# Performance work log

Measured on AMD Instinct MI355X. Metric: run time of the kernel, lower is better.

The kernel has to match this reference:

```python
import jax, jax.numpy as jnp
import numpy as np

N = 20000
E = 320000
F_IN = 256
NHID = 64
H1 = 8
H2 = 1
NUM_CLASSES = 40
NEG_SLOPE = 0.2


def setup_inputs() -> dict:
    key = jax.random.key(0)
    ks = jax.random.split(key, 11)
    glorot = lambda k, shape: jax.random.normal(k, shape, jnp.float32) * jnp.sqrt(2.0 / (shape[0] + shape[-1]))
    x = jax.random.normal(ks[0], (N, F_IN), jnp.float32)
    edge_index = jax.random.randint(ks[1], (2, E), 0, N, jnp.int64)
    W1 = glorot(ks[2], (F_IN, H1 * NHID))
    att_src1 = glorot(ks[3], (H1, NHID))
    att_dst1 = glorot(ks[4], (H1, NHID))
    b1 = jnp.zeros((H1 * NHID,), jnp.float32)
    W2 = glorot(ks[5], (H1 * NHID, H2 * NUM_CLASSES))
    att_src2 = glorot(ks[6], (H2, NUM_CLASSES))
    att_dst2 = glorot(ks[7], (H2, NUM_CLASSES))
    b2 = jnp.zeros((NUM_CLASSES,), jnp.float32)
    return {"x": x, "edge_index": edge_index, "W1": W1, "att_src1": att_src1,
            "att_dst1": att_dst1, "b1": b1, "W2": W2, "att_src2": att_src2,
            "att_dst2": att_dst2, "b2": b2}


def gat_conv(x, src, dst, W, a_src, a_dst, bias, concat):
    # x: [N, F_in], src/dst: [E'] (self-loops already appended)
    H, C = a_src.shape
    h = (x @ W).reshape(N, H, C)                       # [N,H,C]
    alpha_src = jnp.sum(h * a_src, axis=-1)            # [N,H]
    alpha_dst = jnp.sum(h * a_dst, axis=-1)            # [N,H]
    e = jax.nn.leaky_relu(alpha_src[src] + alpha_dst[dst], NEG_SLOPE)  # [E',H]
    # segment softmax over incoming edges of each dst node
    emax = jax.lax.stop_gradient(jax.ops.segment_max(e, dst, num_segments=N))
    ee = jnp.exp(e - emax[dst])
    denom = jax.ops.segment_sum(ee, dst, num_segments=N)
    alpha = ee / (denom[dst] + 1e-16)                  # [E',H]
    out = jax.ops.segment_sum(alpha[:, :, None] * h[src], dst, num_segments=N)  # [N,H,C]
    out = out.reshape(N, H * C) if concat else out.mean(axis=1)
    return out + bias


def reference(x, edge_index, W1, att_src1, att_dst1, b1, W2, att_src2, att_dst2, b2):
    # PyG GATConv adds self-loops by default
    loops = jnp.arange(N, dtype=edge_index.dtype)
    src = jnp.concatenate([edge_index[0], loops])
    dst = jnp.concatenate([edge_index[1], loops])
    h = gat_conv(x, src, dst, W1, att_src1, att_dst1, b1, concat=True)   # [N, H1*NHID]
    h = jax.nn.elu(h)
    out = gat_conv(h, src, dst, W2, att_src2, att_dst2, b2, concat=False)  # [N, NUM_CLASSES]
    return jax.nn.log_softmax(out, axis=1)
```

## Files before the change

### kernel.cpp

```cpp
#include <hip/hip_runtime.h>
#include <hip/hip_bf16.h>
#include <math.h>

#define N_NODES 20000
#define MPAD 20096
#define N_EDGES 320000
#define EP (N_EDGES + N_NODES)
#define F_IN 256
#define NHID 64
#define H1 8
#define D1 512
#define NCLS 40
#define NEG_SLOPE 0.2f
#define MAXD 128

typedef __attribute__((ext_vector_type(8))) short bf16x8;
typedef __attribute__((ext_vector_type(4))) float f32x4;

__device__ __forceinline__ float wave_max(float v) {
#pragma unroll
  for (int o = 32; o > 0; o >>= 1) v = fmaxf(v, __shfl_xor(v, o));
  return v;
}
__device__ __forceinline__ float wave_sum(float v) {
#pragma unroll
  for (int o = 32; o > 0; o >>= 1) v += __shfl_xor(v, o);
  return v;
}
__device__ __forceinline__ float bf2f(unsigned short u) {
  union { unsigned int i; float f; } c; c.i = ((unsigned int)u) << 16; return c.f;
}
__device__ __forceinline__ unsigned short f2bf(float f) {
  union { float f; unsigned int i; } c; c.f = f;
  unsigned int x = c.i;
  return (unsigned short)((x + 0x7fffu + ((x >> 16) & 1u)) >> 16);
}
__device__ __forceinline__ float asf(unsigned int u) {
  union { unsigned int i; float f; } c; c.i = u; return c.f;
}
__device__ __forceinline__ float lrelu(float x) { return x > 0.f ? x : NEG_SLOPE * x; }

__device__ __forceinline__ void gload16(const void* g, void* l) {
  __builtin_amdgcn_global_load_lds((const __attribute__((address_space(1))) void*)g,
                                   (__attribute__((address_space(3))) void*)l, 16, 0, 0);
}

#define PB_CONV 2512
#define PB_TW1  (PB_CONV + 32)
#define PB_TW2  (PB_TW1 + 96)
#define PB_ZERO (PB_TW2 + 157)
#define PB_PAD  (PB_ZERO + 24)
__global__ __launch_bounds__(256) void prep_kernel(const float* __restrict__ x,
                                                   const float* __restrict__ W1,
                                                   const float* __restrict__ W2,
                                                   unsigned short* __restrict__ xb,
                                                   unsigned short* __restrict__ wb1t,
                                                   unsigned short* __restrict__ wb2t,
                                                   int* __restrict__ deg,
                                                   int* __restrict__ cursor,
                                                   unsigned short* __restrict__ out1b) {
  __shared__ float tsh[64][65];
  int bid = blockIdx.x;
  int t = threadIdx.x;
  if (bid < PB_CONV) {
    size_t base = ((size_t)bid * 256 + t) * 8;
    int row = (int)(base >> 8);
    ushort4 o0, o1;
    if (row < N_NODES) {
      float4 v0 = *(const float4*)&x[base];
      float4 v1 = *(const float4*)&x[base + 4];
      o0 = make_ushort4(f2bf(v0.x), f2bf(v0.y), f2bf(v0.z), f2bf(v0.w));
      o1 = make_ushort4(f2bf(v1.x), f2bf(v1.y), f2bf(v1.z), f2bf(v1.w));
    } else {
      o0 = make_ushort4(0, 0, 0, 0); o1 = o0;
    }
    *(ushort4*)&xb[base] = o0;
    *(ushort4*)&xb[base + 4] = o1;
  } else if (bid < PB_TW1) {
    int b2 = bid - PB_CONV;
    int bk = b2 & 3, bn = b2 >> 2;
    int tr = t >> 4, tc4 = (t & 15) * 4;
#pragma unroll
    for (int i = 0; i < 4; ++i) {
      int k = i * 16 + tr;
      float4 v = *(const float4*)&W1[(size_t)(bk * 64 + k) * D1 + bn * 64 + tc4];
      tsh[k][tc4] = v.x; tsh[k][tc4 + 1] = v.y; tsh[k][tc4 + 2] = v.z; tsh[k][tc4 + 3] = v.w;
    }
    __syncthreads();
#pragma unroll
    for (int i = 0; i < 4; ++i) {
      int n = i * 16 + tr;
      ushort4 o = make_ushort4(f2bf(tsh[tc4][n]), f2bf(tsh[tc4 + 1][n]),
                               f2bf(tsh[tc4 + 2][n]), f2bf(tsh[tc4 + 3][n]));
      *(ushort4*)&wb1t[(size_t)(bn * 64 + n) * F_IN + bk * 64 + tc4] = o;
    }
  } else if (bid < PB_TW2) {
    int idx = (bid - PB_TW1) * 256 + t;
    int c = idx >> 9, k = idx & 511;
    wb2t[idx] = f2bf((c < NCLS) ? W2[(size_t)k * NCLS + c] : 0.f);
  } else if (bid < PB_ZERO) {
    int idx = (bid - PB_TW2) * 256 + t;
    if (idx < N_NODES) deg[idx] = 0;
    else if (idx < 2 * N_NODES) cursor[idx - N_NODES] = 0;
  } else {
    int idx = (bid - PB_ZERO) * 256 + t;
    uint4 z = make_uint4(0, 0, 0, 0);
    *(uint4*)((char*)out1b + (size_t)N_NODES * D1 * 2 + (size_t)idx * 16) = z;
  }
}

__global__ void count_deg(const int* __restrict__ ei, int* __restrict__ deg) {
  int e = blockIdx.x * blockDim.x + threadIdx.x;
  if (e >= EP) return;
  int dst = (e < N_EDGES) ? ei[N_EDGES + e] : (e - N_EDGES);
  atomicAdd(&deg[dst], 1);
}

#define SCAN_T 256
#define SCAN_CHUNK 79
__global__ void scan_kernel(const int* __restrict__ deg, int* __restrict__ offsets) {
  __shared__ int sums[SCAN_T];
  int t = threadIdx.x;
  int lo = t * SCAN_CHUNK;
  int hi = min(lo + SCAN_CHUNK, N_NODES);
  int s = 0;
  for (int i = lo; i < hi; ++i) s += deg[i];
  sums[t] = s;
  __syncthreads();
  if (t == 0) {
    int run = 0;
    for (int i = 0; i < SCAN_T; ++i) { int v = sums[i]; sums[i] = run; run += v; }
  }
  __syncthreads();
  int run = sums[t];
  for (int i = lo; i < hi; ++i) { offsets[i] = run; run += deg[i]; }
  if (hi == N_NODES) offsets[N_NODES] = run;
}

__global__ void scatter_edges(const int* __restrict__ ei, const int* __restrict__ offsets,
                              int* __restrict__ cursor, int* __restrict__ edge_src) {
  int e = blockIdx.x * blockDim.x + threadIdx.x;
  if (e >= EP) return;
  int src, dst;
  if (e < N_EDGES) { src = ei[e]; dst = ei[N_EDGES + e]; }
  else             { src = dst = e - N_EDGES; }
  int pos = offsets[dst] + atomicAdd(&cursor[dst], 1);
  edge_src[pos] = src;
}

__global__ __launch_bounds__(256) void gemm1_mfma(const unsigned short* __restrict__ xb,
                                                  const unsigned short* __restrict__ wb1t,
                                                  const float* __restrict__ a_src,
                                                  const float* __restrict__ a_dst,
                                                  unsigned short* __restrict__ h1b,
                                                  float* __restrict__ asrc,
                                                  float* __restrict__ adst) {
  __shared__ unsigned short As[128 * 32];
  __shared__ unsigned short Bs[128 * 32];
  int tid = threadIdx.x;
  int w = tid >> 6, lane = tid & 63;
  int bn = blockIdx.x & 3, bm = blockIdx.x >> 2;
  int row0 = bm * 128, col0 = bn * 128;
  int wr = w >> 1, wc = w & 1;
  int cl = lane & 15, hi = lane >> 4;
  f32x4 acc[4][4] = {};
  for (int k0 = 0; k0 < F_IN; k0 += 32) {
#pragma unroll
    for (int c = 0; c < 2; ++c) {
      int slot = c * 256 + tid;
      int r = slot >> 2;
      int q = (slot & 3) ^ ((slot >> 3) & 3);
      gload16(xb + (size_t)(row0 + r) * F_IN + k0 + q * 8, (char*)As + (c * 256 + w * 64) * 16);
      gload16(wb1t + (size_t)(col0 + r) * F_IN + k0 + q * 8, (char*)Bs + (c * 256 + w * 64) * 16);
    }
    __syncthreads();
    bf16x8 a[4], b[4];
#pragma unroll
    for (int m = 0; m < 4; ++m) {
      int r = wr * 64 + m * 16 + cl;
      a[m] = *(const bf16x8*)&As[r * 32 + ((hi ^ ((r >> 1) & 3)) << 3)];
    }
#pragma unroll
    for (int n = 0; n < 4; ++n) {
      int r = wc * 64 + n * 16 + cl;
      b[n] = *(const bf16x8*)&Bs[r * 32 + ((hi ^ ((r >> 1) & 3)) << 3)];
    }
#pragma unroll
    for (int m = 0; m < 4; ++m)
#pragma unroll
      for (int n = 0; n < 4; ++n)
        acc[m][n] = __builtin_amdgcn_mfma_f32_16x16x32_bf16(a[m], b[n], acc[m][n], 0, 0, 0);
    __syncthreads();
  }
  int head = bn * 2 + wc;
  float asv[4], adv[4];
#pragma unroll
  for (int n = 0; n < 4; ++n) {
    asv[n] = a_src[head * 64 + n * 16 + cl];
    adv[n] = a_dst[head * 64 + n * 16 + cl];
  }
#pragma unroll
  for (int m = 0; m < 4; ++m) {
#pragma unroll
    for (int r = 0; r < 4; ++r) {
      int grow = row0 + wr * 64 + m * 16 + hi * 4 + r;
      float ps = acc[m][0][r] * asv[0] + acc[m][1][r] * asv[1] +
                 acc[m][2][r] * asv[2] + acc[m][3][r] * asv[3];
      float pd = acc[m][0][r] * adv[0] + acc[m][1][r] * adv[1] +
                 acc[m][2][r] * adv[2] + acc[m][3][r] * adv[3];
#pragma unroll
      for (int o = 8; o > 0; o >>= 1) { ps += __shfl_xor(ps, o); pd += __shfl_xor(pd, o); }
      if (grow < N_NODES) {
#pragma unroll
        for (int n = 0; n < 4; ++n)
          h1b[(size_t)grow * D1 + col0 + wc * 64 + n * 16 + cl] = f2bf(acc[m][n][r]);
        if (cl == 0) { asrc[grow * H1 + head] = ps; adst[grow * H1 + head] = pd; }
      }
    }
  }
}

__global__ __launch_bounds__(128) void agg1_kernel(const int* __restrict__ offsets,
                                                   const int* __restrict__ edge_src,
                                                   const float* __restrict__ asrc,
                                                   const float* __restrict__ adst,
                                                   const unsigned short* __restrict__ h1b,
                                                   const float* __restrict__ b1,
                                                   unsigned short* __restrict__ out1b) {
  __shared__ float alphaT[MAXD][H1 + 1];
  __shared__ int   lsoff[MAXD];
  __shared__ float red[2][8];
  __shared__ float minv[2][8];
  __shared__ float accs[2][D1];
  int n = blockIdx.x;
  int t = threadIdx.x;
  int w = t >> 6, lane = t & 63;
  int base = offsets[n];
  int deg = offsets[n + 1] - base;
  int degc = min(deg, MAXD);

  for (int e = t; e < degc; e += 128) lsoff[e] = edge_src[base + e] << 10;
  __syncthreads();

  int h = t & 7;
  int et = t >> 3;
  float advv = adst[n * H1 + h];
  float m = -INFINITY;
  for (int e = et; e < degc; e += 16) {
    int s = lsoff[e] >> 10;
    float ev = lrelu(asrc[s * H1 + h] + advv);
    alphaT[e][h] = ev;
    m = fmaxf(m, ev);
  }
  for (int e = MAXD + et; e < deg; e += 16)
    m = fmaxf(m, lrelu(asrc[edge_src[base + e] * H1 + h] + advv));
  m = fmaxf(m, __shfl_xor(m, 8));
  m = fmaxf(m, __shfl_xor(m, 16));
  m = fmaxf(m, __shfl_xor(m, 32));
  if (lane < 8) red[w][lane] = m;
  __syncthreads();
  m = fmaxf(red[0][h], red[1][h]);
  float ss = 0.f;
  for (int e = et; e < degc; e += 16) ss += __expf(alphaT[e][h] - m);
  for (int e = MAXD + et; e < deg; e += 16)
    ss += __expf(lrelu(asrc[edge_src[base + e] * H1 + h] + advv) - m);
  ss += __shfl_xor(ss, 8);
  ss += __shfl_xor(ss, 16);
  ss += __shfl_xor(ss, 32);
  __syncthreads();
  if (lane < 8) red[w][lane] = ss;
  __syncthreads();
  float inv = 1.f / (red[0][h] + red[1][h] + 1e-16f);
  if (t < 8) { minv[0][t] = m; minv[1][t] = inv; }
  for (int e = et; e < degc; e += 16)
    alphaT[e][h] = __expf(alphaT[e][h] - m) * inv;
  __syncthreads();

  int myh = lane >> 3;
  const char* hb = (const char*)h1b + lane * 16;
  float acc[8] = {};
  for (int e = w; e < degc; e += 2) {
    float a = alphaT[e][myh];
    uint4 uv = *(const uint4*)(hb + lsoff[e]);
#pragma unroll
    for (int j = 0; j < 4; ++j) {
      unsigned int u = ((const unsigned int*)&uv)[j];
      acc[2 * j]     += a * asf(u << 16);
      acc[2 * j + 1] += a * asf(u & 0xffff0000u);
    }
  }
  if (deg > MAXD) {
    float mh = minv[0][myh], invh = minv[1][myh];
    float advh = adst[n * H1 + myh];
    for (int e = MAXD + w; e < deg; e += 2) {
      int s = edge_src[base + e];
      float a = __expf(lrelu(asrc[s * H1 + myh] + advh) - mh) * invh;
      uint4 uv = *(const uint4*)(hb + ((size_t)s << 10));
#pragma unroll
      for (int j = 0; j < 4; ++j) {
        unsigned int u = ((const unsigned int*)&uv)[j];
        acc[2 * j]     += a * asf(u << 16);
        acc[2 * j + 1] += a * asf(u & 0xffff0000u);
      }
    }
  }
  *(float4*)&accs[w][lane * 8]     = make_float4(acc[0], acc[1], acc[2], acc[3]);
  *(float4*)&accs[w][lane * 8 + 4] = make_float4(acc[4], acc[5], acc[6], acc[7]);
  __syncthreads();

  int c0 = t * 4;
  float4 s0 = *(float4*)&accs[0][c0];
  float4 s1 = *(float4*)&accs[1][c0];
  float4 bv = *(const float4*)&b1[c0];
  float v0 = s0.x + s1.x + bv.x, v1 = s0.y + s1.y + bv.y;
  float v2 = s0.z + s1.z + bv.z, v3 = s0.w + s1.w + bv.w;
  v0 = v0 > 0.f ? v0 : (__expf(v0) - 1.f);
  v1 = v1 > 0.f ? v1 : (__expf(v1) - 1.f);
  v2 = v2 > 0.f ? v2 : (__expf(v2) - 1.f);
  v3 = v3 > 0.f ? v3 : (__expf(v3) - 1.f);
  ushort4 o = make_ushort4(f2bf(v0), f2bf(v1), f2bf(v2), f2bf(v3));
  *(ushort4*)&out1b[(size_t)n * D1 + c0] = o;
}

__global__ __launch_bounds__(256) void gemm2_mfma(const unsigned short* __restrict__ ab,
                                                  const unsigned short* __restrict__ wb2t,
                                                  const float* __restrict__ a_src2,
                                                  const float* __restrict__ a_dst2,
                                                  float* __restrict__ h2,
                                                  float* __restrict__ asrc,
                                                  float* __restrict__ adst) {
  __shared__ unsigned short As[128 * 32];
  __shared__ unsigned short Bs[48 * 32];
  int tid = threadIdx.x;
  int w = tid >> 6, lane = tid & 63;
  int row0 = blockIdx.x * 128;
  int cl = lane & 15, hi = lane >> 4;
  f32x4 acc[2][3] = {};
  for (int k0 = 0; k0 < D1; k0 += 32) {
#pragma unroll
    for (int c = 0; c < 2; ++c) {
      int slot = c * 256 + tid;
      int r = slot >> 2;
      int q = (slot & 3) ^ ((slot >> 3) & 3);
      gload16(ab + (size_t)(row0 + r) * D1 + k0 + q * 8, (char*)As + (c * 256 + w * 64) * 16);
    }
    if (tid < 192) {
      int r = tid >> 2;
      int q = (tid & 3) ^ ((tid >> 3) & 3);
      gload16(wb2t + (size_t)r * D1 + k0 + q * 8, (char*)Bs + w * 64 * 16);
    }
    __syncthreads();
    bf16x8 a[2], b[3];
#pragma unroll
    for (int m = 0; m < 2; ++m) {
      int r = w * 32 + m * 16 + cl;
      a[m] = *(const bf16x8*)&As[r * 32 + ((hi ^ ((r >> 1) & 3)) << 3)];
    }
#pragma unroll
    for (int n = 0; n < 3; ++n) {
      int r = n * 16 + cl;
      b[n] = *(const bf16x8*)&Bs[r * 32 + ((hi ^ ((r >> 1) & 3)) << 3)];
    }
#pragma unroll
    for (int m = 0; m < 2; ++m)
#pragma unroll
      for (int n = 0; n < 3; ++n)
        acc[m][n] = __builtin_amdgcn_mfma_f32_16x16x32_bf16(a[m], b[n], acc[m][n], 0, 0, 0);
    __syncthreads();
  }
  float asv[3], adv[3];
#pragma unroll
  for (int n = 0; n < 3; ++n) {
    int c = n * 16 + cl;
    asv[n] = (c < NCLS) ? a_src2[c] : 0.f;
    adv[n] = (c < NCLS) ? a_dst2[c] : 0.f;
  }
#pragma unroll
  for (int m = 0; m < 2; ++m) {
#pragma unroll
    for (int r = 0; r < 4; ++r) {
      int grow = row0 + w * 32 + m * 16 + hi * 4 + r;
      float ps = acc[m][0][r] * asv[0] + acc[m][1][r] * asv[1] + acc[m][2][r] * asv[2];
      float pd = acc[m][0][r] * adv[0] + acc[m][1][r] * adv[1] + acc[m][2][r] * adv[2];
#pragma unroll
      for (int o = 8; o > 0; o >>= 1) { ps += __shfl_xor(ps, o); pd += __shfl_xor(pd, o); }
      if (grow < N_NODES) {
#pragma unroll
        for (int n = 0; n < 3; ++n) {
          int c = n * 16 + cl;
          if (c < NCLS) h2[(size_t)grow * NCLS + c] = acc[m][n][r];
        }
        if (cl == 0) { asrc[grow] = ps; adst[grow] = pd; }
      }
    }
  }
}

__global__ __launch_bounds__(256) void agg2_kernel(const int* __restrict__ offsets,
                                                   const int* __restrict__ edge_src,
                                                   const float* __restrict__ asrc,
                                                   const float* __restrict__ adst,
                                                   const float* __restrict__ h2,
                                                   const float* __restrict__ b2,
                                                   float* __restrict__ out) {
  __shared__ float lalpha[4][MAXD];
  __shared__ int   lsoff[4][MAXD];
  int w = threadIdx.x >> 6;
  int lane = threadIdx.x & 63;
  int n = blockIdx.x * 4 + w;
  int base = offsets[n];
  int deg = offsets[n + 1] - base;
  int degc = min(deg, MAXD);
  int degp = ((degc + 2) / 3) * 3;

  float advv = adst[n];
  float m = -INFINITY;
  for (int e = lane; e < deg; e += 64) {
    int s = edge_src[base + e];
    float ev = lrelu(asrc[s] + advv);
    if (e < MAXD) { lsoff[w][e] = s * (NCLS * 4); lalpha[w][e] = ev; }
    m = fmaxf(m, ev);
  }
  m = wave_max(m);
  float ssum = 0.f;
  for (int e = lane; e < deg; e += 64) {
    float ev;
    if (e < MAXD) ev = lalpha[w][e];
    else { int s = edge_src[base + e]; ev = lrelu(asrc[s] + advv); }
    ssum += __expf(ev - m);
  }
  float inv = 1.f / (wave_sum(ssum) + 1e-16f);
  for (int e = lane; e < degc; e += 64) lalpha[w][e] = __expf(lalpha[w][e] - m) * inv;
  {
    int e = degc + lane;
    if (e < degp && e < MAXD) { lalpha[w][e] = 0.f; lsoff[w][e] = 0; }
  }

  int esub = lane / 20;
  int cg = lane - esub * 20;
  bool act = esub < 3;
  float ax = 0.f, ay = 0.f;
  const char* hb = (const char*)h2 + cg * 8;
  for (int i = 0; i < degp; i += 3) {
    if (act) {
      int slot = i + esub;
      float a = lalpha[w][slot];
      int so = lsoff[w][slot];
      float2 hv = *(const float2*)(hb + so);
      ax += a * hv.x; ay += a * hv.y;
    }
  }
  for (int e = MAXD + esub; e < deg; e += 3) {
    if (act) {
      int s = edge_src[base + e];
      float a = __expf(lrelu(asrc[s] + advv) - m) * inv;
      float2 hv = *(const float2*)(hb + (size_t)s * (NCLS * 4));
      ax += a * hv.x; ay += a * hv.y;
    }
  }
  float ax1 = __shfl(ax, lane + 20), ax2 = __shfl(ax, lane + 40);
  float ay1 = __shfl(ay, lane + 20), ay2 = __shfl(ay, lane + 40);
  float v0 = -INFINITY, v1 = -INFINITY;
  if (lane < 20) {
    v0 = ax + ax1 + ax2 + b2[2 * cg];
    v1 = ay + ay1 + ay2 + b2[2 * cg + 1];
  }
  float m2 = wave_max(fmaxf(v0, v1));
  float se = wave_sum(lane < 20 ? __expf(v0 - m2) + __expf(v1 - m2) : 0.f);
  if (lane < 20) {
    float ls = logf(se);
    *(float2*)&out[(size_t)n * NCLS + 2 * cg] = make_float2(v0 - m2 - ls, v1 - m2 - ls);
  }
}

extern "C" void kernel_launch(void* const* d_in, const int* in_sizes, int n_in,
                              void* d_out, int out_size, void* d_ws, size_t ws_size,
                              hipStream_t stream) {
  const float* x   = (const float*)d_in[0];
  const int*   ei  = (const int*)d_in[1];
  const float* W1  = (const float*)d_in[2];
  const float* as1 = (const float*)d_in[3];
  const float* ad1 = (const float*)d_in[4];
  const float* b1  = (const float*)d_in[5];
  const float* W2  = (const float*)d_in[6];
  const float* as2 = (const float*)d_in[7];
  const float* ad2 = (const float*)d_in[8];
  const float* b2  = (const float*)d_in[9];
  float* out = (float*)d_out;

  char* ws = (char*)d_ws;
  size_t off = 0;
  auto alloc = [&](size_t bytes) -> char* {
    char* p = ws + off;
    off += (bytes + 255) & ~(size_t)255;
    return p;
  };
  int* deg      = (int*)alloc((size_t)N_NODES * 4);
  int* cursor   = (int*)alloc((size_t)N_NODES * 4);
  int* offsets  = (int*)alloc((size_t)(N_NODES + 1) * 4);
  int* edge_src = (int*)alloc((size_t)EP * 4);
  unsigned short* xb    = (unsigned short*)alloc((size_t)MPAD * F_IN * 2);
  unsigned short* wb1t  = (unsigned short*)alloc((size_t)D1 * F_IN * 2);
  unsigned short* wb2t  = (unsigned short*)alloc((size_t)48 * D1 * 2);
  unsigned short* h1b   = (unsigned short*)alloc((size_t)N_NODES * D1 * 2);
  unsigned short* out1b = (unsigned short*)alloc((size_t)MPAD * D1 * 2);
  float* asrc1  = (float*)alloc((size_t)N_NODES * H1 * 4);
  float* adst1  = (float*)alloc((size_t)N_NODES * H1 * 4);
  float* h2     = (float*)alloc((size_t)N_NODES * NCLS * 4);
  float* asrc2  = (float*)alloc((size_t)N_NODES * 4);
  float* adst2  = (float*)alloc((size_t)N_NODES * 4);

  prep_kernel<<<PB_PAD, 256, 0, stream>>>(x, W1, W2, xb, wb1t, wb2t, deg, cursor, out1b);
  count_deg<<<(EP + 255) / 256, 256, 0, stream>>>(ei, deg);
  scan_kernel<<<1, SCAN_T, 0, stream>>>(deg, offsets);
  scatter_edges<<<(EP + 255) / 256, 256, 0, stream>>>(ei, offsets, cursor, edge_src);

  gemm1_mfma<<<157 * 4, 256, 0, stream>>>(xb, wb1t, as1, ad1, h1b, asrc1, adst1);
  agg1_kernel<<<N_NODES, 128, 0, stream>>>(offsets, edge_src, asrc1, adst1, h1b, b1, out1b);

  gemm2_mfma<<<157, 256, 0, stream>>>(out1b, wb2t, as2, ad2, h2, asrc2, adst2);
  agg2_kernel<<<N_NODES / 4, 256, 0, stream>>>(offsets, edge_src, asrc2, adst2, h2, b2, out);
}
```

Measured before the change: 172.6 us.

## Parallelize scan, widen GEMM K-tiles, shrink gemm2 rows, unroll agg1 gather

The degree scan now runs on 1024 threads and uses wavefront shuffle prefix sums in place of a serial 256-entry loop. Both GEMMs move from 32 to 64 K per tile with a new XOR swizzle, halving the barrier and load iterations. gemm2 uses 64-row blocks for more workgroups. The agg1 gather loop is unrolled by two to keep more loads in flight. These changes add shared memory use and register pressure.

```diff
diff --git a/kernel.cpp b/kernel.cpp
--- a/kernel.cpp
+++ b/kernel.cpp
@@ -116,25 +116,34 @@
   atomicAdd(&deg[dst], 1);
 }
 
-#define SCAN_T 256
-#define SCAN_CHUNK 79
-__global__ void scan_kernel(const int* __restrict__ deg, int* __restrict__ offsets) {
-  __shared__ int sums[SCAN_T];
+#define SCAN_T 1024
+#define SCAN_CHUNK 20
+__global__ __launch_bounds__(1024) void scan_kernel(const int* __restrict__ deg,
+                                                    int* __restrict__ offsets) {
+  __shared__ int wsum[16];
   int t = threadIdx.x;
+  int w = t >> 6, lane = t & 63;
   int lo = t * SCAN_CHUNK;
   int hi = min(lo + SCAN_CHUNK, N_NODES);
   int s = 0;
   for (int i = lo; i < hi; ++i) s += deg[i];
-  sums[t] = s;
+  int incl = s;
+#pragma unroll
+  for (int o = 1; o < 64; o <<= 1) {
+    int v = __shfl_up(incl, o);
+    if (lane >= o) incl += v;
+  }
+  if (lane == 63) wsum[w] = incl;
   __syncthreads();
   if (t == 0) {
     int run = 0;
-    for (int i = 0; i < SCAN_T; ++i) { int v = sums[i]; sums[i] = run; run += v; }
-  }
-  __syncthreads();
-  int run = sums[t];
-  for (int i = lo; i < hi; ++i) { offsets[i] = run; run += deg[i]; }
-  if (hi == N_NODES) offsets[N_NODES] = run;
+#pragma unroll
+    for (int i = 0; i < 16; ++i) { int v = wsum[i]; wsum[i] = run; run += v; }
+  }
+  __syncthreads();
+  int off = wsum[w] + incl - s;
+  for (int i = lo; i < hi; ++i) { offsets[i] = off; off += deg[i]; }
+  if (hi == N_NODES && lo < N_NODES) offsets[N_NODES] = off;
 }
 
 __global__ void scatter_edges(const int* __restrict__ ei, const int* __restrict__ offsets,
@@ -155,8 +164,8 @@
                                                   unsigned short* __restrict__ h1b,
                                                   float* __restrict__ asrc,
                                                   float* __restrict__ adst) {
-  __shared__ unsigned short As[128 * 32];
-  __shared__ unsigned short Bs[128 * 32];
+  __shared__ unsigned short As[128 * 64];
+  __shared__ unsigned short Bs[128 * 64];
   int tid = threadIdx.x;
   int w = tid >> 6, lane = tid & 63;
   int bn = blockIdx.x & 3, bm = blockIdx.x >> 2;
@@ -164,32 +173,35 @@
   int wr = w >> 1, wc = w & 1;
   int cl = lane & 15, hi = lane >> 4;
   f32x4 acc[4][4] = {};
-  for (int k0 = 0; k0 < F_IN; k0 += 32) {
-#pragma unroll
-    for (int c = 0; c < 2; ++c) {
+  for (int k0 = 0; k0 < F_IN; k0 += 64) {
+#pragma unroll
+    for (int c = 0; c < 4; ++c) {
       int slot = c * 256 + tid;
-      int r = slot >> 2;
-      int q = (slot & 3) ^ ((slot >> 3) & 3);
+      int r = slot >> 3;
+      int q = (slot & 7) ^ (r & 7);
       gload16(xb + (size_t)(row0 + r) * F_IN + k0 + q * 8, (char*)As + (c * 256 + w * 64) * 16);
       gload16(wb1t + (size_t)(col0 + r) * F_IN + k0 + q * 8, (char*)Bs + (c * 256 + w * 64) * 16);
     }
     __syncthreads();
-    bf16x8 a[4], b[4];
-#pragma unroll
-    for (int m = 0; m < 4; ++m) {
-      int r = wr * 64 + m * 16 + cl;
-      a[m] = *(const bf16x8*)&As[r * 32 + ((hi ^ ((r >> 1) & 3)) << 3)];
-    }
-#pragma unroll
-    for (int n = 0; n < 4; ++n) {
-      int r = wc * 64 + n * 16 + cl;
-      b[n] = *(const bf16x8*)&Bs[r * 32 + ((hi ^ ((r >> 1) & 3)) << 3)];
-    }
-#pragma unroll
-    for (int m = 0; m < 4; ++m)
-#pragma unroll
-      for (int n = 0; n < 4; ++n)
-        acc[m][n] = __builtin_amdgcn_mfma_f32_16x16x32_bf16(a[m], b[n], acc[m][n], 0, 0, 0);
+#pragma unroll
+    for (int kk = 0; kk < 2; ++kk) {
+      bf16x8 a[4], b[4];
+#pragma unroll
+      for (int m = 0; m < 4; ++m) {
+        int r = wr * 64 + m * 16 + cl;
+        a[m] = *(const bf16x8*)&As[r * 64 + ((((kk * 4 + hi)) ^ (r & 7)) << 3)];
+      }
+#pragma unroll
+      for (int n = 0; n < 4; ++n) {
+        int r = wc * 64 + n * 16 + cl;
+        b[n] = *(const bf16x8*)&Bs[r * 64 + ((((kk * 4 + hi)) ^ (r & 7)) << 3)];
+      }
+#pragma unroll
+      for (int m = 0; m < 4; ++m)
+#pragma unroll
+        for (int n = 0; n < 4; ++n)
+          acc[m][n] = __builtin_amdgcn_mfma_f32_16x16x32_bf16(a[m], b[n], acc[m][n], 0, 0, 0);
+    }
     __syncthreads();
   }
   int head = bn * 2 + wc;
@@ -279,7 +291,23 @@
   int myh = lane >> 3;
   const char* hb = (const char*)h1b + lane * 16;
   float acc[8] = {};
-  for (int e = w; e < degc; e += 2) {
+  int e = w;
+  for (; e + 2 < degc; e += 4) {
+    float a0 = alphaT[e][myh];
+    float a1 = alphaT[e + 2][myh];
+    uint4 u0 = *(const uint4*)(hb + lsoff[e]);
+    uint4 u1 = *(const uint4*)(hb + lsoff[e + 2]);
+#pragma unroll
+    for (int j = 0; j < 4; ++j) {
+      unsigned int x0 = ((const unsigned int*)&u0)[j];
+      unsigned int x1 = ((const unsigned int*)&u1)[j];
+      acc[2 * j]     += a0 * asf(x0 << 16);
+      acc[2 * j + 1] += a0 * asf(x0 & 0xffff0000u);
+      acc[2 * j]     += a1 * asf(x1 << 16);
+      acc[2 * j + 1] += a1 * asf(x1 & 0xffff0000u);
+    }
+  }
+  for (; e < degc; e += 2) {
     float a = alphaT[e][myh];
     uint4 uv = *(const uint4*)(hb + lsoff[e]);
 #pragma unroll
@@ -292,8 +320,8 @@
   if (deg > MAXD) {
     float mh = minv[0][myh], invh = minv[1][myh];
     float advh = adst[n * H1 + myh];
-    for (int e = MAXD + w; e < deg; e += 2) {
-      int s = edge_src[base + e];
+    for (int e2 = MAXD + w; e2 < deg; e2 += 2) {
+      int s = edge_src[base + e2];
       float a = __expf(lrelu(asrc[s * H1 + myh] + advh) - mh) * invh;
       uint4 uv = *(const uint4*)(hb + ((size_t)s << 10));
 #pragma unroll
@@ -329,43 +357,44 @@
                                                   float* __restrict__ h2,
                                                   float* __restrict__ asrc,
                                                   float* __restrict__ adst) {
-  __shared__ unsigned short As[128 * 32];
-  __shared__ unsigned short Bs[48 * 32];
+  __shared__ unsigned short As[64 * 64];
+  __shared__ unsigned short Bs[48 * 64];
   int tid = threadIdx.x;
   int w = tid >> 6, lane = tid & 63;
-  int row0 = blockIdx.x * 128;
+  int row0 = blockIdx.x * 64;
   int cl = lane & 15, hi = lane >> 4;
-  f32x4 acc[2][3] = {};
-  for (int k0 = 0; k0 < D1; k0 += 32) {
+  f32x4 acc[3] = {};
+  for (int k0 = 0; k0 < D1; k0 += 64) {
 #pragma unroll
     for (int c = 0; c < 2; ++c) {
       int slot = c * 256 + tid;
-      int r = slot >> 2;
-      int q = (slot & 3) ^ ((slot >> 3) & 3);
+      int r = slot >> 3;
+      int q = (slot & 7) ^ (r & 7);
       gload16(ab + (size_t)(row0 + r) * D1 + k0 + q * 8, (char*)As + (c * 256 + w * 64) * 16);
     }
-    if (tid < 192) {
-      int r = tid >> 2;
-      int q = (tid & 3) ^ ((tid >> 3) & 3);
-      gload16(wb2t + (size_t)r * D1 + k0 + q * 8, (char*)Bs + w * 64 * 16);
+    {
+      int r = tid >> 3;
+      int q = (tid & 7) ^ (r & 7);
+      gload16(wb2t + (size_t)r * D1 + k0 + q * 8, (char*)Bs + (w * 64) * 16);
+      if (tid < 128) {
+        int slot2 = 256 + tid;
+        int r2 = slot2 >> 3;
+        int q2 = (slot2 & 7) ^ (r2 & 7);
+        gload16(wb2t + (size_t)r2 * D1 + k0 + q2 * 8, (char*)Bs + ((256 + w * 64)) * 16);
+      }
     }
     __syncthreads();
-    bf16x8 a[2], b[3];
-#pragma unroll
-    for (int m = 0; m < 2; ++m) {
-      int r = w * 32 + m * 16 + cl;
-      a[m] = *(const bf16x8*)&As[r * 32 + ((hi ^ ((r >> 1) & 3)) << 3)];
-    }
-#pragma unroll
-    for (int n = 0; n < 3; ++n) {
-      int r = n * 16 + cl;
-      b[n] = *(const bf16x8*)&Bs[r * 32 + ((hi ^ ((r >> 1) & 3)) << 3)];
-    }
-#pragma unroll
-    for (int m = 0; m < 2; ++m)
-#pragma unroll
-      for (int n = 0; n < 3; ++n)
-        acc[m][n] = __builtin_amdgcn_mfma_f32_16x16x32_bf16(a[m], b[n], acc[m][n], 0, 0, 0);
+#pragma unroll
+    for (int kk = 0; kk < 2; ++kk) {
+      int ra = w * 16 + cl;
+      bf16x8 a = *(const bf16x8*)&As[ra * 64 + (((kk * 4 + hi) ^ (ra & 7)) << 3)];
+#pragma unroll
+      for (int n = 0; n < 3; ++n) {
+        int rb = n * 16 + cl;
+        bf16x8 b = *(const bf16x8*)&Bs[rb * 64 + (((kk * 4 + hi) ^ (rb & 7)) << 3)];
+        acc[n] = __builtin_amdgcn_mfma_f32_16x16x32_bf16(a, b, acc[n], 0, 0, 0);
+      }
+    }
     __syncthreads();
   }
   float asv[3], adv[3];
@@ -376,22 +405,19 @@
     adv[n] = (c < NCLS) ? a_dst2[c] : 0.f;
   }
 #pragma unroll
-  for (int m = 0; m < 2; ++m) {
-#pragma unroll
-    for (int r = 0; r < 4; ++r) {
-      int grow = row0 + w * 32 + m * 16 + hi * 4 + r;
-      float ps = acc[m][0][r] * asv[0] + acc[m][1][r] * asv[1] + acc[m][2][r] * asv[2];
-      float pd = acc[m][0][r] * adv[0] + acc[m][1][r] * adv[1] + acc[m][2][r] * adv[2];
-#pragma unroll
-      for (int o = 8; o > 0; o >>= 1) { ps += __shfl_xor(ps, o); pd += __shfl_xor(pd, o); }
-      if (grow < N_NODES) {
-#pragma unroll
-        for (int n = 0; n < 3; ++n) {
-          int c = n * 16 + cl;
-          if (c < NCLS) h2[(size_t)grow * NCLS + c] = acc[m][n][r];
-        }
-        if (cl == 0) { asrc[grow] = ps; adst[grow] = pd; }
-      }
+  for (int r = 0; r < 4; ++r) {
+    int grow = row0 + w * 16 + hi * 4 + r;
+    float ps = acc[0][r] * asv[0] + acc[1][r] * asv[1] + acc[2][r] * asv[2];
+    float pd = acc[0][r] * adv[0] + acc[1][r] * adv[1] + acc[2][r] * adv[2];
+#pragma unroll
+    for (int o = 8; o > 0; o >>= 1) { ps += __shfl_xor(ps, o); pd += __shfl_xor(pd, o); }
+    if (grow < N_NODES) {
+#pragma unroll
+      for (int n = 0; n < 3; ++n) {
+        int c = n * 16 + cl;
+        if (c < NCLS) h2[(size_t)grow * NCLS + c] = acc[n][r];
+      }
+      if (cl == 0) { asrc[grow] = ps; adst[grow] = pd; }
     }
   }
 }
@@ -518,6 +544,6 @@
   gemm1_mfma<<<157 * 4, 256, 0, stream>>>(xb, wb1t, as1, ad1, h1b, asrc1, adst1);
   agg1_kernel<<<N_NODES, 128, 0, stream>>>(offsets, edge_src, asrc1, adst1, h1b, b1, out1b);
 
-  gemm2_mfma<<<157, 256, 0, stream>>>(out1b, wb2t, as2, ad2, h2, asrc2, adst2);
+  gemm2_mfma<<<MPAD / 64, 256, 0, stream>>>(out1b, wb2t, as2, ad2, h2, asrc2, adst2);
   agg2_kernel<<<N_NODES / 4, 256, 0, stream>>>(offsets, edge_src, asrc2, adst2, h2, b2, out);
 }
```

Result: faster. 159.3 us (-7.7%).
